# Performance work log

Hardware: AMD Instinct MI355X
Metric: run time of the kernel (lower is better)

## Reference

```python
import jax, jax.numpy as jnp
import numpy as np
import math

B, N, H, TDIM, K, R = 32, 4096, 256, 128, 2, 2


def setup_inputs() -> dict:
    key = jax.random.key(0)
    ks = jax.random.split(key, 12)
    s = 1.0 / math.sqrt(H)
    gain = 1.414
    return {
        "x": jax.random.normal(ks[0], (B, N), jnp.float32),
        "t": jax.random.uniform(ks[1], (B,), jnp.float32),
        # scaled so repeated L@x stays O(1) over Chebyshev hops
        "laplacian": jax.random.normal(ks[2], (N, N), jnp.float32) / math.sqrt(N),
        "w_g1": jax.random.normal(ks[3], (1, H, K + 1), jnp.float32) * gain / math.sqrt(1 + H),
        "w_g2": jax.random.normal(ks[4], (H, 1, K + 1), jnp.float32) * gain / math.sqrt(1 + H),
        "w_t1": jax.random.normal(ks[5], (TDIM, H), jnp.float32) / math.sqrt(TDIM),
        "b_t1": jnp.zeros((H,), jnp.float32),
        "w_t2": jax.random.normal(ks[6], (H, H), jnp.float32) * s,
        "b_t2": jnp.zeros((H,), jnp.float32),
        "w_map": jax.random.normal(ks[7], (N, H), jnp.float32) / math.sqrt(N),
        "b_map": jnp.zeros((H,), jnp.float32),
        "res_w": jax.random.normal(ks[8], (R, 3, H, H), jnp.float32) * s,
        "res_b": jnp.zeros((R, 3, H), jnp.float32),
        "w_o1": jax.random.normal(ks[9], (H, H), jnp.float32) * s,
        "b_o1": jnp.zeros((H,), jnp.float32),
        "w_o2": jax.random.normal(ks[10], (H, N), jnp.float32) * s,
        "b_o2": jnp.zeros((N,), jnp.float32),
    }


def timestep_embedding(t, dim, max_period=10000):
    half = dim // 2  # dim is even here
    freqs = jnp.exp(-math.log(max_period) * jnp.arange(half, dtype=t.dtype) / half)
    args = t[:, None] * freqs[None, :]  # [B, half]
    return jnp.concatenate([jnp.cos(args), jnp.sin(args)], axis=-1)  # [B, dim]


def gcn_layer(L, x, w, conv_order):
    xs = [x]
    h = x
    for _ in range(conv_order):
        h = jnp.einsum('mn,bnc->bmc', L, h)  # sparse-style Laplacian propagation (dense here)
        xs.append(h)
    X = jnp.stack(xs, axis=-1)  # [B, N, C, K+1]
    return jnp.einsum('bnik,iok->bno', X, w)


def reference(x, t, laplacian, w_g1, w_g2, w_t1, b_t1, w_t2, b_t2,
              w_map, b_map, res_w, res_b, w_o1, b_o1, w_o2, b_o2):
    silu = jax.nn.silu
    # time embedding path: sinusoidal -> Linear -> SiLU -> Linear
    temb = timestep_embedding(t, TDIM)
    t_out = silu(temb @ w_t1 + b_t1) @ w_t2 + b_t2  # [B, H]
    # GCNBlock: two Chebyshev GCN layers (GCNLayer.forward applies no activation)
    g = gcn_layer(laplacian, x[:, :, None], w_g1, K)  # [B, N, H]
    g = gcn_layer(laplacian, g, w_g2, K)[..., 0]      # [B, N]
    # ResNet_FC on the node signal
    h = g @ w_map + b_map  # [B, H]
    inv_sqrt2 = 1.0 / math.sqrt(2.0)
    for r in range(R):
        z = h
        for i in range(3):
            z = silu(z @ res_w[r, i] + res_b[r, i])
        h = (h + z) * inv_sqrt2
    # output head with time conditioning
    out = silu((h + t_out) @ w_o1 + b_o1) @ w_o2 + b_o2  # [B, N]
    return out
```

## Files before the change

kernel.cpp:

```cpp
#include <hip/hip_runtime.h>
#include <hip/hip_bf16.h>

typedef __bf16 bf16x8 __attribute__((ext_vector_type(8)));
typedef __bf16 bf16x4 __attribute__((ext_vector_type(4)));
typedef float  f32x4  __attribute__((ext_vector_type(4)));


static constexpr size_t WS_A     = 0;
static constexpr size_t WS_TOUT  = 1024;
static constexpr size_t WS_H0    = 65536;
static constexpr size_t WS_UB    = 131072;
static constexpr size_t WS_XB    = 262144;
static constexpr size_t WS_G2B   = 524288;
static constexpr size_t WS_ZB1   = 1048576;
static constexpr size_t WS_ZBSTR = 262144;
static constexpr size_t WS_Z1    = 2097152;
static constexpr size_t WS_ZSTR  = 524288;
static constexpr size_t WS_WMAPT = 4194304;
static constexpr size_t WS_WO2T  = 6291456;
static constexpr size_t WS_LB    = 8388608;

__device__ __forceinline__ f32x4 mfma16(bf16x8 a, bf16x8 b, f32x4 c) {
    return __builtin_amdgcn_mfma_f32_16x16x32_bf16(a, b, c, 0, 0, 0);
}

__device__ __forceinline__ bf16x8 cvt8(const float* p) {
    f32x4 lo = *(const f32x4*)p;
    f32x4 hi = *(const f32x4*)(p + 4);
    bf16x8 r;
    r[0] = (__bf16)lo[0]; r[1] = (__bf16)lo[1]; r[2] = (__bf16)lo[2]; r[3] = (__bf16)lo[3];
    r[4] = (__bf16)hi[0]; r[5] = (__bf16)hi[1]; r[6] = (__bf16)hi[2]; r[7] = (__bf16)hi[3];
    return r;
}

__device__ __forceinline__ float silu_f(float x) { return x / (1.0f + __expf(-x)); }

__device__ __forceinline__ void transpose_tile(const float* __restrict__ src, int sstride,
                                               __bf16* __restrict__ dst, int dstride,
                                               int r0, int c0, float* sh, int tid) {
    const int r = tid >> 3, cg = (tid & 7) * 4;
    f32x4 v = *(const f32x4*)(src + (size_t)(r0 + r) * sstride + c0 + cg);
    sh[r * 33 + cg + 0] = v[0];
    sh[r * 33 + cg + 1] = v[1];
    sh[r * 33 + cg + 2] = v[2];
    sh[r * 33 + cg + 3] = v[3];
    __syncthreads();
    bf16x4 o;
    o[0] = (__bf16)sh[(cg + 0) * 33 + r];
    o[1] = (__bf16)sh[(cg + 1) * 33 + r];
    o[2] = (__bf16)sh[(cg + 2) * 33 + r];
    o[3] = (__bf16)sh[(cg + 3) * 33 + r];
    *(bf16x4*)(dst + (size_t)(c0 + r) * dstride + r0 + cg) = o;
}

__global__ __launch_bounds__(256) void prep_kernel(
    const float* __restrict__ x, const float* __restrict__ t,
    const float* __restrict__ w_g1, const float* __restrict__ w_g2,
    const float* __restrict__ w_t1, const float* __restrict__ b_t1,
    const float* __restrict__ w_t2, const float* __restrict__ b_t2,
    const float* __restrict__ w_map, const float* __restrict__ w_o2,
    char* __restrict__ ws)
{
    __shared__ float sh[1056];
    const int bi = blockIdx.x, tid = threadIdx.x;
    if (bi == 0) {
        const float g10 = w_g1[tid * 3 + 0], g11 = w_g1[tid * 3 + 1], g12 = w_g1[tid * 3 + 2];
        const float g20 = w_g2[tid * 3 + 0], g21 = w_g2[tid * 3 + 1], g22 = w_g2[tid * 3 + 2];
        float p[9] = {g10 * g20, g10 * g21, g10 * g22,
                      g11 * g20, g11 * g21, g11 * g22,
                      g12 * g20, g12 * g21, g12 * g22};
        const int wv = tid >> 6, ln = tid & 63;
#pragma unroll
        for (int j = 0; j < 9; ++j) {
            float v = p[j];
#pragma unroll
            for (int off = 32; off > 0; off >>= 1) v += __shfl_down(v, off);
            if (ln == 0) sh[wv * 9 + j] = v;
        }
        __syncthreads();
        if (tid == 0) {
            float s[9];
#pragma unroll
            for (int j = 0; j < 9; ++j) s[j] = sh[j] + sh[9 + j] + sh[18 + j] + sh[27 + j];
            float* a = (float*)(ws + WS_A);
            a[0] = s[0];
            a[1] = s[1] + s[3];
            a[2] = s[2] + s[4] + s[6];
            a[3] = s[5] + s[7];
            a[4] = s[8];
        }
    } else if (bi < 33) {
        const int b = bi - 1;
        float* t_out = (float*)(ws + WS_TOUT);
        if (tid < 64) {
            float fr = __expf(-9.210340371976184f * (float)tid * (1.0f / 64.0f));
            float ang = t[b] * fr;
            sh[tid]      = __cosf(ang);
            sh[64 + tid] = __sinf(ang);
        }
        __syncthreads();
        float acc = b_t1[tid];
        for (int j = 0; j < 128; ++j) acc += sh[j] * w_t1[j * 256 + tid];
        sh[128 + tid] = silu_f(acc);
        __syncthreads();
        float acc2 = b_t2[tid];
        for (int j = 0; j < 256; ++j) acc2 += sh[128 + j] * w_t2[j * 256 + tid];
        t_out[b * 256 + tid] = acc2;
    } else if (bi < 41) {
        f32x4* p = (f32x4*)(ws + WS_H0);
        f32x4 z = {0.f, 0.f, 0.f, 0.f};
        p[(bi - 33) * 256 + tid] = z;
    } else if (bi < 105) {
        const int e = ((bi - 41) * 256 + tid) * 8;
        *(bf16x8*)((__bf16*)(ws + WS_XB) + e) = cvt8(x + e);
    } else if (bi < 1129) {
        const int ti = bi - 105;
        transpose_tile(w_map, 256, (__bf16*)(ws + WS_WMAPT), 4096,
                       (ti >> 3) * 32, (ti & 7) * 32, sh, tid);
    } else {
        const int ti = bi - 1129;
        transpose_tile(w_o2, 4096, (__bf16*)(ws + WS_WO2T), 256,
                       (ti & 7) * 32, (ti >> 3) * 32, sh, tid);
    }
}

__global__ __launch_bounds__(1024) void hop1_kernel(
    const float* __restrict__ L, const __bf16* __restrict__ xb,
    float* __restrict__ zout, __bf16* __restrict__ zb_out,
    __bf16* __restrict__ Lb)
{
    __shared__ float red[16][16][33];
    const int bi = blockIdx.x, tid = threadIdx.x;
    const int wave = tid >> 6, lane = tid & 63;
    const int l15 = lane & 15, q = lane >> 4;
    const int m0 = bi * 16;
    const int kbase = wave * 256;

    const float*  lp  = L  + (size_t)(m0 + l15) * 4096;
    __bf16*       lbp = Lb + (size_t)(m0 + l15) * 4096;
    const __bf16* b0p = xb + (size_t)l15 * 4096;
    const __bf16* b1p = xb + (size_t)(l15 + 16) * 4096;

    f32x4 acc0 = {0,0,0,0}, acc1 = {0,0,0,0};
#pragma unroll
    for (int ks = 0; ks < 8; ++ks) {
        const int k = kbase + ks * 32 + q * 8;
        bf16x8 a  = cvt8(lp + k);
        *(bf16x8*)(lbp + k) = a;
        bf16x8 b0 = *(const bf16x8*)(b0p + k);
        bf16x8 b1 = *(const bf16x8*)(b1p + k);
        acc0 = mfma16(a, b0, acc0);
        acc1 = mfma16(a, b1, acc1);
    }
#pragma unroll
    for (int r = 0; r < 4; ++r) {
        red[wave][q * 4 + r][l15]      = acc0[r];
        red[wave][q * 4 + r][l15 + 16] = acc1[r];
    }
    __syncthreads();
    if (tid < 512) {
        const int m = tid & 15, b = tid >> 4;
        float v = 0.f;
#pragma unroll
        for (int w = 0; w < 16; ++w) v += red[w][m][b];
        zout[(size_t)b * 4096 + m0 + m] = v;
        zb_out[(size_t)b * 4096 + m0 + m] = (__bf16)v;
    }
}

__global__ __launch_bounds__(1024) void hop_bf_kernel(
    const __bf16* __restrict__ Lb, const __bf16* __restrict__ zb_in,
    float* __restrict__ zout, __bf16* __restrict__ zb_out)
{
    __shared__ float red[16][16][33];
    const int bi = blockIdx.x, tid = threadIdx.x;
    const int wave = tid >> 6, lane = tid & 63;
    const int l15 = lane & 15, q = lane >> 4;
    const int m0 = bi * 16;
    const int kbase = wave * 256;

    const __bf16* ap  = Lb + (size_t)(m0 + l15) * 4096;
    const __bf16* b0p = zb_in + (size_t)l15 * 4096;
    const __bf16* b1p = zb_in + (size_t)(l15 + 16) * 4096;

    f32x4 acc0 = {0,0,0,0}, acc1 = {0,0,0,0};
#pragma unroll
    for (int ks = 0; ks < 8; ++ks) {
        const int k = kbase + ks * 32 + q * 8;
        bf16x8 a  = *(const bf16x8*)(ap + k);
        bf16x8 b0 = *(const bf16x8*)(b0p + k);
        bf16x8 b1 = *(const bf16x8*)(b1p + k);
        acc0 = mfma16(a, b0, acc0);
        acc1 = mfma16(a, b1, acc1);
    }
#pragma unroll
    for (int r = 0; r < 4; ++r) {
        red[wave][q * 4 + r][l15]      = acc0[r];
        red[wave][q * 4 + r][l15 + 16] = acc1[r];
    }
    __syncthreads();
    if (tid < 512) {
        const int m = tid & 15, b = tid >> 4;
        float v = 0.f;
#pragma unroll
        for (int w = 0; w < 16; ++w) v += red[w][m][b];
        zout[(size_t)b * 4096 + m0 + m] = v;
        if (zb_out) zb_out[(size_t)b * 4096 + m0 + m] = (__bf16)v;
    }
}

__global__ __launch_bounds__(256) void combine_kernel(
    const float* __restrict__ x,
    const float* __restrict__ z1, const float* __restrict__ z2,
    const float* __restrict__ z3, const float* __restrict__ z4,
    const float* __restrict__ a, __bf16* __restrict__ g2b)
{
    const int i = blockIdx.x * 256 + threadIdx.x;
    const float a0 = a[0], a1 = a[1], a2 = a[2], a3 = a[3], a4 = a[4];
    f32x4 r = a0 * ((const f32x4*)x)[i] + a1 * ((const f32x4*)z1)[i]
            + a2 * ((const f32x4*)z2)[i] + a3 * ((const f32x4*)z3)[i]
            + a4 * ((const f32x4*)z4)[i];
    bf16x4 o;
    o[0] = (__bf16)r[0]; o[1] = (__bf16)r[1]; o[2] = (__bf16)r[2]; o[3] = (__bf16)r[3];
    ((bf16x4*)g2b)[i] = o;
}

__global__ __launch_bounds__(256) void map_gemm_kernel(
    const __bf16* __restrict__ g2b, const __bf16* __restrict__ w_mapT,
    float* __restrict__ h0)
{
    __shared__ float red[4][16][32];
    const int bi = blockIdx.x, tid = threadIdx.x;
    const int wave = tid >> 6, lane = tid & 63;
    const int l15 = lane & 15, q = lane >> 4;
    const int btile = bi & 1;
    const int hp = (bi >> 1) & 7;
    const int kc = bi >> 4;
    const int kbase = kc * 512 + wave * 128;

    const __bf16* ap  = g2b + (size_t)(btile * 16 + l15) * 4096;
    const __bf16* bp0 = w_mapT + (size_t)(hp * 32 + l15) * 4096;
    const __bf16* bp1 = w_mapT + (size_t)(hp * 32 + 16 + l15) * 4096;

    f32x4 acc0 = {0,0,0,0}, acc1 = {0,0,0,0};
#pragma unroll
    for (int ks = 0; ks < 4; ++ks) {
        const int k = kbase + ks * 32 + q * 8;
        bf16x8 a  = *(const bf16x8*)(ap + k);
        bf16x8 b0 = *(const bf16x8*)(bp0 + k);
        bf16x8 b1 = *(const bf16x8*)(bp1 + k);
        acc0 = mfma16(a, b0, acc0);
        acc1 = mfma16(a, b1, acc1);
    }
#pragma unroll
    for (int r = 0; r < 4; ++r) {
        red[wave][q * 4 + r][l15]      = acc0[r];
        red[wave][q * 4 + r][l15 + 16] = acc1[r];
    }
    __syncthreads();
    const int b_l = tid >> 4, hl = tid & 15;
#pragma unroll
    for (int s = 0; s < 2; ++s) {
        const int h_l = hl + s * 16;
        float v = red[0][b_l][h_l] + red[1][b_l][h_l] + red[2][b_l][h_l] + red[3][b_l][h_l];
        atomicAdd(h0 + (size_t)(btile * 16 + b_l) * 256 + hp * 32 + h_l, v);
    }
}

__global__ __launch_bounds__(1024) void resnet_kernel(
    const float* __restrict__ h0, const float* __restrict__ b_map,
    const float* __restrict__ res_w, const float* __restrict__ res_b,
    const float* __restrict__ t_out, const float* __restrict__ w_o1,
    const float* __restrict__ b_o1, __bf16* __restrict__ u_b)
{
    __shared__ float zs[256];
    __shared__ float part[4][256];
    const int b = blockIdx.x, tid = threadIdx.x;
    const int col = tid & 255, kg = tid >> 8;

    float hv = 0.f;
    if (kg == 0) {
        hv = h0[b * 256 + col] + b_map[col];
        zs[col] = hv;
    }
    __syncthreads();

#pragma unroll
    for (int r = 0; r < 2; ++r) {
        for (int i = 0; i < 3; ++i) {
            const float* W = res_w + ((size_t)(r * 3 + i) << 16) + (size_t)kg * 64 * 256 + col;
            const float* zp = zs + kg * 64;
            float a0 = 0, a1 = 0, a2 = 0, a3 = 0;
#pragma unroll
            for (int j = 0; j < 64; j += 4) {
                a0 += zp[j]     * W[(j)     * 256];
                a1 += zp[j + 1] * W[(j + 1) * 256];
                a2 += zp[j + 2] * W[(j + 2) * 256];
                a3 += zp[j + 3] * W[(j + 3) * 256];
            }
            part[kg][col] = (a0 + a1) + (a2 + a3);
            __syncthreads();
            if (kg == 0) {
                zs[col] = silu_f(res_b[(r * 3 + i) * 256 + col]
                                 + part[0][col] + part[1][col] + part[2][col] + part[3][col]);
            }
            __syncthreads();
        }
        if (kg == 0) {
            hv = (hv + zs[col]) * 0.70710678118654752f;
            zs[col] = hv;
        }
        __syncthreads();
    }

    if (kg == 0) zs[col] = hv + t_out[b * 256 + col];
    __syncthreads();
    {
        const float* W = w_o1 + (size_t)kg * 64 * 256 + col;
        const float* zp = zs + kg * 64;
        float a0 = 0, a1 = 0, a2 = 0, a3 = 0;
#pragma unroll
        for (int j = 0; j < 64; j += 4) {
            a0 += zp[j]     * W[(j)     * 256];
            a1 += zp[j + 1] * W[(j + 1) * 256];
            a2 += zp[j + 2] * W[(j + 2) * 256];
            a3 += zp[j + 3] * W[(j + 3) * 256];
        }
        part[kg][col] = (a0 + a1) + (a2 + a3);
    }
    __syncthreads();
    if (kg == 0) {
        u_b[b * 256 + col] = (__bf16)silu_f(b_o1[col]
            + part[0][col] + part[1][col] + part[2][col] + part[3][col]);
    }
}

__global__ __launch_bounds__(256) void out_gemm_kernel(
    const __bf16* __restrict__ u_b, const __bf16* __restrict__ w_o2T,
    const float* __restrict__ b_o2, float* __restrict__ out)
{
    const int tid = threadIdx.x;
    const int wave = tid >> 6, lane = tid & 63;
    const int l15 = lane & 15, q = lane >> 4;
    const int g = blockIdx.x * 4 + wave;
    const int btile = g & 1;
    const int n0 = (g >> 1) * 32;

    const __bf16* ap  = u_b + (size_t)(btile * 16 + l15) * 256;
    const __bf16* bp0 = w_o2T + (size_t)(n0 + l15) * 256;
    const __bf16* bp1 = w_o2T + (size_t)(n0 + 16 + l15) * 256;

    f32x4 acc0 = {0,0,0,0}, acc1 = {0,0,0,0};
#pragma unroll
    for (int ks = 0; ks < 8; ++ks) {
        const int k = ks * 32 + q * 8;
        bf16x8 a  = *(const bf16x8*)(ap + k);
        bf16x8 b0 = *(const bf16x8*)(bp0 + k);
        bf16x8 b1 = *(const bf16x8*)(bp1 + k);
        acc0 = mfma16(a, b0, acc0);
        acc1 = mfma16(a, b1, acc1);
    }
    const int row = btile * 16 + q * 4;
    const int na = n0 + l15, nb = n0 + 16 + l15;
#pragma unroll
    for (int r = 0; r < 4; ++r) {
        out[(size_t)(row + r) * 4096 + na] = acc0[r] + b_o2[na];
        out[(size_t)(row + r) * 4096 + nb] = acc1[r] + b_o2[nb];
    }
}

extern "C" void kernel_launch(void* const* d_in, const int* in_sizes, int n_in,
                              void* d_out, int out_size, void* d_ws, size_t ws_size,
                              hipStream_t stream)
{
    (void)in_sizes; (void)n_in; (void)out_size; (void)ws_size;
    const float* x     = (const float*)d_in[0];
    const float* t     = (const float*)d_in[1];
    const float* L     = (const float*)d_in[2];
    const float* w_g1  = (const float*)d_in[3];
    const float* w_g2  = (const float*)d_in[4];
    const float* w_t1  = (const float*)d_in[5];
    const float* b_t1  = (const float*)d_in[6];
    const float* w_t2  = (const float*)d_in[7];
    const float* b_t2  = (const float*)d_in[8];
    const float* w_map = (const float*)d_in[9];
    const float* b_map = (const float*)d_in[10];
    const float* res_w = (const float*)d_in[11];
    const float* res_b = (const float*)d_in[12];
    const float* w_o1  = (const float*)d_in[13];
    const float* b_o1  = (const float*)d_in[14];
    const float* w_o2  = (const float*)d_in[15];
    const float* b_o2  = (const float*)d_in[16];
    float* out = (float*)d_out;
    char* ws = (char*)d_ws;

    float*  a_c  = (float*)(ws + WS_A);
    float*  tout = (float*)(ws + WS_TOUT);
    float*  h0   = (float*)(ws + WS_H0);
    __bf16* u_b  = (__bf16*)(ws + WS_UB);
    __bf16* xb   = (__bf16*)(ws + WS_XB);
    __bf16* g2b  = (__bf16*)(ws + WS_G2B);
    __bf16* zb1  = (__bf16*)(ws + WS_ZB1);
    __bf16* zb2  = (__bf16*)(ws + WS_ZB1 + WS_ZBSTR);
    __bf16* zb3  = (__bf16*)(ws + WS_ZB1 + 2 * WS_ZBSTR);
    float*  z1   = (float*)(ws + WS_Z1);
    float*  z2   = (float*)(ws + WS_Z1 + WS_ZSTR);
    float*  z3   = (float*)(ws + WS_Z1 + 2 * WS_ZSTR);
    float*  z4   = (float*)(ws + WS_Z1 + 3 * WS_ZSTR);
    __bf16* w_mapT = (__bf16*)(ws + WS_WMAPT);
    __bf16* w_o2T  = (__bf16*)(ws + WS_WO2T);
    __bf16* Lb     = (__bf16*)(ws + WS_LB);

    prep_kernel<<<2153, 256, 0, stream>>>(x, t, w_g1, w_g2, w_t1, b_t1, w_t2, b_t2,
                                          w_map, w_o2, ws);
    hop1_kernel<<<256, 1024, 0, stream>>>(L, xb, z1, zb1, Lb);
    hop_bf_kernel<<<256, 1024, 0, stream>>>(Lb, zb1, z2, zb2);
    hop_bf_kernel<<<256, 1024, 0, stream>>>(Lb, zb2, z3, zb3);
    hop_bf_kernel<<<256, 1024, 0, stream>>>(Lb, zb3, z4, nullptr);
    combine_kernel<<<128, 256, 0, stream>>>(x, z1, z2, z3, z4, a_c, g2b);
    map_gemm_kernel<<<128, 256, 0, stream>>>(g2b, w_mapT, h0);
    resnet_kernel<<<32, 1024, 0, stream>>>(h0, b_map, res_w, res_b, tout, w_o1, b_o1, u_b);
    out_gemm_kernel<<<64, 256, 0, stream>>>(u_b, w_o2T, b_o2, out);
}
```

Measured before the change: 229.2 us.

## Fuse Chebyshev hops, combine and map GEMM into one persistent kernel with grid barriers

Six kernels (four Laplacian hops, the combine step and the map GEMM) become one persistent 256-block kernel. Each block keeps its 16-row slice of L in LDS as swizzled bf16, so L is read from HBM once and never written back as a bf16 copy. Hop results stay in registers, and the hops are separated by atomic-counter grid barriers. This removes launch gaps, the round trips of the Lb copy and the fp32 z buffers, and the separate combine pass. The risks are deadlock if all 256 blocks are not co-resident, since 128KB of LDS is used per block, and the cost of the spin barriers.

```diff
diff --git a/kernel.cpp b/kernel.cpp
--- a/kernel.cpp
+++ b/kernel.cpp
@@ -7,18 +7,15 @@
 
 
 static constexpr size_t WS_A     = 0;
+static constexpr size_t WS_BAR   = 512;
 static constexpr size_t WS_TOUT  = 1024;
 static constexpr size_t WS_H0    = 65536;
 static constexpr size_t WS_UB    = 131072;
 static constexpr size_t WS_XB    = 262144;
 static constexpr size_t WS_G2B   = 524288;
-static constexpr size_t WS_ZB1   = 1048576;
-static constexpr size_t WS_ZBSTR = 262144;
-static constexpr size_t WS_Z1    = 2097152;
-static constexpr size_t WS_ZSTR  = 524288;
+static constexpr size_t WS_ZB    = 1048576;
 static constexpr size_t WS_WMAPT = 4194304;
 static constexpr size_t WS_WO2T  = 6291456;
-static constexpr size_t WS_LB    = 8388608;
 
 __device__ __forceinline__ f32x4 mfma16(bf16x8 a, bf16x8 b, f32x4 c) {
     return __builtin_amdgcn_mfma_f32_16x16x32_bf16(a, b, c, 0, 0, 0);
@@ -107,6 +104,7 @@
         for (int j = 0; j < 256; ++j) acc2 += sh[128 + j] * w_t2[j * 256 + tid];
         t_out[b * 256 + tid] = acc2;
     } else if (bi < 41) {
+        if (bi == 33 && tid == 0) *(unsigned*)(ws + WS_BAR) = 0u;
         f32x4* p = (f32x4*)(ws + WS_H0);
         f32x4 z = {0.f, 0.f, 0.f, 0.f};
         p[(bi - 33) * 256 + tid] = z;
@@ -124,146 +122,149 @@
     }
 }
 
-__global__ __launch_bounds__(1024) void hop1_kernel(
-    const float* __restrict__ L, const __bf16* __restrict__ xb,
-    float* __restrict__ zout, __bf16* __restrict__ zb_out,
-    __bf16* __restrict__ Lb)
+__device__ __forceinline__ void gbar(unsigned* bar, unsigned target) {
+    __syncthreads();
+    if (threadIdx.x == 0) {
+        __threadfence();
+        __hip_atomic_fetch_add(bar, 1u, __ATOMIC_RELEASE, __HIP_MEMORY_SCOPE_AGENT);
+        while (__hip_atomic_load(bar, __ATOMIC_RELAXED, __HIP_MEMORY_SCOPE_AGENT) < target)
+            __builtin_amdgcn_s_sleep(2);
+        (void)__hip_atomic_load(bar, __ATOMIC_ACQUIRE, __HIP_MEMORY_SCOPE_AGENT);
+    }
+    __syncthreads();
+}
+
+__global__ __launch_bounds__(1024) void cheb_fused(
+    const float* __restrict__ L, const float* __restrict__ x, char* __restrict__ ws)
 {
-    __shared__ float red[16][16][33];
+    __shared__ __bf16 lb[16 * 4096];
+    __shared__ float red[8][16][33];
+
+    unsigned* bar        = (unsigned*)(ws + WS_BAR);
+    const float* a_c     = (const float*)(ws + WS_A);
+    const __bf16* xb     = (const __bf16*)(ws + WS_XB);
+    const __bf16* w_mapT = (const __bf16*)(ws + WS_WMAPT);
+    __bf16* g2b          = (__bf16*)(ws + WS_G2B);
+    __bf16* zb1          = (__bf16*)(ws + WS_ZB);
+    __bf16* zb2          = zb1 + 131072;
+    __bf16* zb3          = zb2 + 131072;
+    float* h0            = (float*)(ws + WS_H0);
+
     const int bi = blockIdx.x, tid = threadIdx.x;
     const int wave = tid >> 6, lane = tid & 63;
     const int l15 = lane & 15, q = lane >> 4;
     const int m0 = bi * 16;
-    const int kbase = wave * 256;
-
-    const float*  lp  = L  + (size_t)(m0 + l15) * 4096;
-    __bf16*       lbp = Lb + (size_t)(m0 + l15) * 4096;
-    const __bf16* b0p = xb + (size_t)l15 * 4096;
-    const __bf16* b1p = xb + (size_t)(l15 + 16) * 4096;
-
-    f32x4 acc0 = {0,0,0,0}, acc1 = {0,0,0,0};
-#pragma unroll
-    for (int ks = 0; ks < 8; ++ks) {
-        const int k = kbase + ks * 32 + q * 8;
-        bf16x8 a  = cvt8(lp + k);
-        *(bf16x8*)(lbp + k) = a;
-        bf16x8 b0 = *(const bf16x8*)(b0p + k);
-        bf16x8 b1 = *(const bf16x8*)(b1p + k);
-        acc0 = mfma16(a, b0, acc0);
-        acc1 = mfma16(a, b1, acc1);
-    }
-#pragma unroll
-    for (int r = 0; r < 4; ++r) {
-        red[wave][q * 4 + r][l15]      = acc0[r];
-        red[wave][q * 4 + r][l15 + 16] = acc1[r];
-    }
-    __syncthreads();
+
+    {
+        const int cb = tid * 8;
+#pragma unroll
+        for (int i = 0; i < 16; ++i) {
+            f32x4 v = *(const f32x4*)(L + (size_t)(m0 + i) * 4096 + tid * 4);
+            bf16x4 o;
+            o[0] = (__bf16)v[0]; o[1] = (__bf16)v[1];
+            o[2] = (__bf16)v[2]; o[3] = (__bf16)v[3];
+            *(bf16x4*)((char*)lb + i * 8192 + (cb ^ ((i & 7) << 4))) = o;
+        }
+    }
+    __syncthreads();
+
+    const int xr = (l15 & 7) << 4;
+    const char* arow = (const char*)lb + l15 * 8192;
+    const int kb0 = wave * 512 + q * 16;
+
+    float z1v, z2v, z3v, z4v;
+
+    auto hop = [&](const __bf16* bsrc, __bf16* zb_out, float& zv) {
+        const __bf16* b0p = bsrc + (size_t)l15 * 4096;
+        const __bf16* b1p = bsrc + (size_t)(l15 + 16) * 4096;
+        f32x4 acc0 = {0,0,0,0}, acc1 = {0,0,0,0};
+#pragma unroll
+        for (int ks = 0; ks < 8; ++ks) {
+            const int kbyte = kb0 + ks * 64;
+            bf16x8 a = *(const bf16x8*)(arow + (kbyte ^ xr));
+            const int k = kbyte >> 1;
+            bf16x8 b0 = *(const bf16x8*)(b0p + k);
+            bf16x8 b1 = *(const bf16x8*)(b1p + k);
+            acc0 = mfma16(a, b0, acc0);
+            acc1 = mfma16(a, b1, acc1);
+        }
+        if (wave >= 8) {
+#pragma unroll
+            for (int r = 0; r < 4; ++r) {
+                red[wave - 8][q * 4 + r][l15]      = acc0[r];
+                red[wave - 8][q * 4 + r][l15 + 16] = acc1[r];
+            }
+        }
+        __syncthreads();
+        if (wave < 8) {
+#pragma unroll
+            for (int r = 0; r < 4; ++r) {
+                red[wave][q * 4 + r][l15]      += acc0[r];
+                red[wave][q * 4 + r][l15 + 16] += acc1[r];
+            }
+        }
+        __syncthreads();
+        float v = 0.f;
+        if (tid < 512) {
+            const int m = tid & 15, b = tid >> 4;
+#pragma unroll
+            for (int w = 0; w < 8; ++w) v += red[w][m][b];
+            if (zb_out) zb_out[(size_t)b * 4096 + m0 + m] = (__bf16)v;
+        }
+        zv = v;
+    };
+
+    hop(xb, zb1, z1v);
+    gbar(bar, 256u);
+    hop(zb1, zb2, z2v);
+    gbar(bar, 512u);
+    hop(zb2, zb3, z3v);
+    gbar(bar, 768u);
+    hop(zb3, nullptr, z4v);
+
     if (tid < 512) {
         const int m = tid & 15, b = tid >> 4;
-        float v = 0.f;
-#pragma unroll
-        for (int w = 0; w < 16; ++w) v += red[w][m][b];
-        zout[(size_t)b * 4096 + m0 + m] = v;
-        zb_out[(size_t)b * 4096 + m0 + m] = (__bf16)v;
-    }
-}
-
-__global__ __launch_bounds__(1024) void hop_bf_kernel(
-    const __bf16* __restrict__ Lb, const __bf16* __restrict__ zb_in,
-    float* __restrict__ zout, __bf16* __restrict__ zb_out)
-{
-    __shared__ float red[16][16][33];
-    const int bi = blockIdx.x, tid = threadIdx.x;
-    const int wave = tid >> 6, lane = tid & 63;
-    const int l15 = lane & 15, q = lane >> 4;
-    const int m0 = bi * 16;
-    const int kbase = wave * 256;
-
-    const __bf16* ap  = Lb + (size_t)(m0 + l15) * 4096;
-    const __bf16* b0p = zb_in + (size_t)l15 * 4096;
-    const __bf16* b1p = zb_in + (size_t)(l15 + 16) * 4096;
-
-    f32x4 acc0 = {0,0,0,0}, acc1 = {0,0,0,0};
-#pragma unroll
-    for (int ks = 0; ks < 8; ++ks) {
-        const int k = kbase + ks * 32 + q * 8;
-        bf16x8 a  = *(const bf16x8*)(ap + k);
-        bf16x8 b0 = *(const bf16x8*)(b0p + k);
-        bf16x8 b1 = *(const bf16x8*)(b1p + k);
-        acc0 = mfma16(a, b0, acc0);
-        acc1 = mfma16(a, b1, acc1);
-    }
-#pragma unroll
-    for (int r = 0; r < 4; ++r) {
-        red[wave][q * 4 + r][l15]      = acc0[r];
-        red[wave][q * 4 + r][l15 + 16] = acc1[r];
-    }
-    __syncthreads();
-    if (tid < 512) {
-        const int m = tid & 15, b = tid >> 4;
-        float v = 0.f;
-#pragma unroll
-        for (int w = 0; w < 16; ++w) v += red[w][m][b];
-        zout[(size_t)b * 4096 + m0 + m] = v;
-        if (zb_out) zb_out[(size_t)b * 4096 + m0 + m] = (__bf16)v;
-    }
-}
-
-__global__ __launch_bounds__(256) void combine_kernel(
-    const float* __restrict__ x,
-    const float* __restrict__ z1, const float* __restrict__ z2,
-    const float* __restrict__ z3, const float* __restrict__ z4,
-    const float* __restrict__ a, __bf16* __restrict__ g2b)
-{
-    const int i = blockIdx.x * 256 + threadIdx.x;
-    const float a0 = a[0], a1 = a[1], a2 = a[2], a3 = a[3], a4 = a[4];
-    f32x4 r = a0 * ((const f32x4*)x)[i] + a1 * ((const f32x4*)z1)[i]
-            + a2 * ((const f32x4*)z2)[i] + a3 * ((const f32x4*)z3)[i]
-            + a4 * ((const f32x4*)z4)[i];
-    bf16x4 o;
-    o[0] = (__bf16)r[0]; o[1] = (__bf16)r[1]; o[2] = (__bf16)r[2]; o[3] = (__bf16)r[3];
-    ((bf16x4*)g2b)[i] = o;
-}
-
-__global__ __launch_bounds__(256) void map_gemm_kernel(
-    const __bf16* __restrict__ g2b, const __bf16* __restrict__ w_mapT,
-    float* __restrict__ h0)
-{
-    __shared__ float red[4][16][32];
-    const int bi = blockIdx.x, tid = threadIdx.x;
-    const int wave = tid >> 6, lane = tid & 63;
-    const int l15 = lane & 15, q = lane >> 4;
-    const int btile = bi & 1;
-    const int hp = (bi >> 1) & 7;
-    const int kc = bi >> 4;
-    const int kbase = kc * 512 + wave * 128;
-
-    const __bf16* ap  = g2b + (size_t)(btile * 16 + l15) * 4096;
-    const __bf16* bp0 = w_mapT + (size_t)(hp * 32 + l15) * 4096;
-    const __bf16* bp1 = w_mapT + (size_t)(hp * 32 + 16 + l15) * 4096;
-
-    f32x4 acc0 = {0,0,0,0}, acc1 = {0,0,0,0};
-#pragma unroll
-    for (int ks = 0; ks < 4; ++ks) {
-        const int k = kbase + ks * 32 + q * 8;
-        bf16x8 a  = *(const bf16x8*)(ap + k);
-        bf16x8 b0 = *(const bf16x8*)(bp0 + k);
-        bf16x8 b1 = *(const bf16x8*)(bp1 + k);
-        acc0 = mfma16(a, b0, acc0);
-        acc1 = mfma16(a, b1, acc1);
-    }
-#pragma unroll
-    for (int r = 0; r < 4; ++r) {
-        red[wave][q * 4 + r][l15]      = acc0[r];
-        red[wave][q * 4 + r][l15 + 16] = acc1[r];
-    }
-    __syncthreads();
-    const int b_l = tid >> 4, hl = tid & 15;
-#pragma unroll
-    for (int s = 0; s < 2; ++s) {
-        const int h_l = hl + s * 16;
-        float v = red[0][b_l][h_l] + red[1][b_l][h_l] + red[2][b_l][h_l] + red[3][b_l][h_l];
-        atomicAdd(h0 + (size_t)(btile * 16 + b_l) * 256 + hp * 32 + h_l, v);
+        const float xv = x[(size_t)b * 4096 + m0 + m];
+        const float g = a_c[0] * xv + a_c[1] * z1v + a_c[2] * z2v
+                      + a_c[3] * z3v + a_c[4] * z4v;
+        g2b[(size_t)b * 4096 + m0 + m] = (__bf16)g;
+    }
+    gbar(bar, 1024u);
+
+    {
+        const int btile = bi & 1, hp = (bi >> 1) & 7, kc = bi >> 4;
+        if (wave < 4) {
+            const int kbase = kc * 256 + wave * 64;
+            const __bf16* ap  = g2b + (size_t)(btile * 16 + l15) * 4096;
+            const __bf16* bp0 = w_mapT + (size_t)(hp * 32 + l15) * 4096;
+            const __bf16* bp1 = w_mapT + (size_t)(hp * 32 + 16 + l15) * 4096;
+            f32x4 acc0 = {0,0,0,0}, acc1 = {0,0,0,0};
+#pragma unroll
+            for (int ks = 0; ks < 2; ++ks) {
+                const int k = kbase + ks * 32 + q * 8;
+                bf16x8 a  = *(const bf16x8*)(ap + k);
+                bf16x8 b0 = *(const bf16x8*)(bp0 + k);
+                bf16x8 b1 = *(const bf16x8*)(bp1 + k);
+                acc0 = mfma16(a, b0, acc0);
+                acc1 = mfma16(a, b1, acc1);
+            }
+#pragma unroll
+            for (int r = 0; r < 4; ++r) {
+                red[wave][q * 4 + r][l15]      = acc0[r];
+                red[wave][q * 4 + r][l15 + 16] = acc1[r];
+            }
+        }
+        __syncthreads();
+        if (tid < 256) {
+            const int b_l = tid >> 4, hl = tid & 15;
+#pragma unroll
+            for (int s = 0; s < 2; ++s) {
+                const int h_l = hl + s * 16;
+                const float v = red[0][b_l][h_l] + red[1][b_l][h_l]
+                              + red[2][b_l][h_l] + red[3][b_l][h_l];
+                atomicAdd(h0 + (size_t)(btile * 16 + b_l) * 256 + hp * 32 + h_l, v);
+            }
+        }
     }
 }
 
@@ -394,31 +395,14 @@
     float* out = (float*)d_out;
     char* ws = (char*)d_ws;
 
-    float*  a_c  = (float*)(ws + WS_A);
     float*  tout = (float*)(ws + WS_TOUT);
     float*  h0   = (float*)(ws + WS_H0);
     __bf16* u_b  = (__bf16*)(ws + WS_UB);
-    __bf16* xb   = (__bf16*)(ws + WS_XB);
-    __bf16* g2b  = (__bf16*)(ws + WS_G2B);
-    __bf16* zb1  = (__bf16*)(ws + WS_ZB1);
-    __bf16* zb2  = (__bf16*)(ws + WS_ZB1 + WS_ZBSTR);
-    __bf16* zb3  = (__bf16*)(ws + WS_ZB1 + 2 * WS_ZBSTR);
-    float*  z1   = (float*)(ws + WS_Z1);
-    float*  z2   = (float*)(ws + WS_Z1 + WS_ZSTR);
-    float*  z3   = (float*)(ws + WS_Z1 + 2 * WS_ZSTR);
-    float*  z4   = (float*)(ws + WS_Z1 + 3 * WS_ZSTR);
-    __bf16* w_mapT = (__bf16*)(ws + WS_WMAPT);
-    __bf16* w_o2T  = (__bf16*)(ws + WS_WO2T);
-    __bf16* Lb     = (__bf16*)(ws + WS_LB);
+    __bf16* w_o2T = (__bf16*)(ws + WS_WO2T);
 
     prep_kernel<<<2153, 256, 0, stream>>>(x, t, w_g1, w_g2, w_t1, b_t1, w_t2, b_t2,
                                           w_map, w_o2, ws);
-    hop1_kernel<<<256, 1024, 0, stream>>>(L, xb, z1, zb1, Lb);
-    hop_bf_kernel<<<256, 1024, 0, stream>>>(Lb, zb1, z2, zb2);
-    hop_bf_kernel<<<256, 1024, 0, stream>>>(Lb, zb2, z3, zb3);
-    hop_bf_kernel<<<256, 1024, 0, stream>>>(Lb, zb3, z4, nullptr);
-    combine_kernel<<<128, 256, 0, stream>>>(x, z1, z2, z3, z4, a_c, g2b);
-    map_gemm_kernel<<<128, 256, 0, stream>>>(g2b, w_mapT, h0);
+    cheb_fused<<<256, 1024, 0, stream>>>(L, x, ws);
     resnet_kernel<<<32, 1024, 0, stream>>>(h0, b_map, res_w, res_b, tout, w_o1, b_o1, u_b);
     out_gemm_kernel<<<64, 256, 0, stream>>>(u_b, w_o2T, b_o2, out);
 }
```

Result: slower. 286.7 us (+25.1%).

## Prefetch hop loads into registers, fuse combine into last hop, vectorize resnet

Applied to the files above, without the earlier changes.

Hop kernels now issue all their global loads up front, or double-buffer them in hop1, so more memory requests are in flight before the MFMAs run. The separate combine kernel is folded into the fourth hop's epilogue, which removes one launch and the write and reread of z4. The resnet kernel is reorganized into 16 k-groups using f32x4 weight loads through a shared layer lambda. Launch bounds with min-blocks hints are added, which raises register pressure from the larger prefetch arrays.

```diff
diff --git a/kernel.cpp b/kernel.cpp
--- a/kernel.cpp
+++ b/kernel.cpp
@@ -12,10 +12,10 @@
 static constexpr size_t WS_UB    = 131072;
 static constexpr size_t WS_XB    = 262144;
 static constexpr size_t WS_G2B   = 524288;
-static constexpr size_t WS_ZB1   = 1048576;
+static constexpr size_t WS_ZB    = 1048576;
 static constexpr size_t WS_ZBSTR = 262144;
-static constexpr size_t WS_Z1    = 2097152;
-static constexpr size_t WS_ZSTR  = 524288;
+static constexpr size_t WS_ZF    = 2097152;
+static constexpr size_t WS_ZFSTR = 524288;
 static constexpr size_t WS_WMAPT = 4194304;
 static constexpr size_t WS_WO2T  = 6291456;
 static constexpr size_t WS_LB    = 8388608;
@@ -124,9 +124,9 @@
     }
 }
 
-__global__ __launch_bounds__(1024) void hop1_kernel(
+__global__ __launch_bounds__(1024, 4) void hop1_kernel(
     const float* __restrict__ L, const __bf16* __restrict__ xb,
-    float* __restrict__ zout, __bf16* __restrict__ zb_out,
+    float* __restrict__ zf_out, __bf16* __restrict__ zb_out,
     __bf16* __restrict__ Lb)
 {
     __shared__ float red[16][16][33];
@@ -134,23 +134,46 @@
     const int wave = tid >> 6, lane = tid & 63;
     const int l15 = lane & 15, q = lane >> 4;
     const int m0 = bi * 16;
-    const int kbase = wave * 256;
+    const int kbase = wave * 256 + q * 8;
 
     const float*  lp  = L  + (size_t)(m0 + l15) * 4096;
     __bf16*       lbp = Lb + (size_t)(m0 + l15) * 4096;
     const __bf16* b0p = xb + (size_t)l15 * 4096;
     const __bf16* b1p = xb + (size_t)(l15 + 16) * 4096;
 
+    f32x4 af0[4], af1[4];
+    bf16x8 b0r[4], b1r[4];
+#pragma unroll
+    for (int p = 0; p < 4; ++p) {
+        const int k = kbase + p * 32;
+        af0[p] = *(const f32x4*)(lp + k);
+        af1[p] = *(const f32x4*)(lp + k + 4);
+        b0r[p] = *(const bf16x8*)(b0p + k);
+        b1r[p] = *(const bf16x8*)(b1p + k);
+    }
+
     f32x4 acc0 = {0,0,0,0}, acc1 = {0,0,0,0};
 #pragma unroll
     for (int ks = 0; ks < 8; ++ks) {
-        const int k = kbase + ks * 32 + q * 8;
-        bf16x8 a  = cvt8(lp + k);
-        *(bf16x8*)(lbp + k) = a;
-        bf16x8 b0 = *(const bf16x8*)(b0p + k);
-        bf16x8 b1 = *(const bf16x8*)(b1p + k);
-        acc0 = mfma16(a, b0, acc0);
-        acc1 = mfma16(a, b1, acc1);
+        const int p = ks & 3;
+        bf16x8 a;
+        a[0] = (__bf16)af0[p][0]; a[1] = (__bf16)af0[p][1];
+        a[2] = (__bf16)af0[p][2]; a[3] = (__bf16)af0[p][3];
+        a[4] = (__bf16)af1[p][0]; a[5] = (__bf16)af1[p][1];
+        a[6] = (__bf16)af1[p][2]; a[7] = (__bf16)af1[p][3];
+        *(bf16x8*)(lbp + kbase + ks * 32) = a;
+        if (ks < 4) {
+            const int k2 = kbase + (ks + 4) * 32;
+            af0[p] = *(const f32x4*)(lp + k2);
+            af1[p] = *(const f32x4*)(lp + k2 + 4);
+            acc0 = mfma16(a, b0r[p], acc0);
+            acc1 = mfma16(a, b1r[p], acc1);
+            b0r[p] = *(const bf16x8*)(b0p + k2);
+            b1r[p] = *(const bf16x8*)(b1p + k2);
+        } else {
+            acc0 = mfma16(a, b0r[p], acc0);
+            acc1 = mfma16(a, b1r[p], acc1);
+        }
     }
 #pragma unroll
     for (int r = 0; r < 4; ++r) {
@@ -163,35 +186,39 @@
         float v = 0.f;
 #pragma unroll
         for (int w = 0; w < 16; ++w) v += red[w][m][b];
-        zout[(size_t)b * 4096 + m0 + m] = v;
+        zf_out[(size_t)b * 4096 + m0 + m] = v;
         zb_out[(size_t)b * 4096 + m0 + m] = (__bf16)v;
     }
 }
 
-__global__ __launch_bounds__(1024) void hop_bf_kernel(
+__global__ __launch_bounds__(1024, 4) void hop_mid_kernel(
     const __bf16* __restrict__ Lb, const __bf16* __restrict__ zb_in,
-    float* __restrict__ zout, __bf16* __restrict__ zb_out)
+    float* __restrict__ zf_out, __bf16* __restrict__ zb_out)
 {
     __shared__ float red[16][16][33];
     const int bi = blockIdx.x, tid = threadIdx.x;
     const int wave = tid >> 6, lane = tid & 63;
     const int l15 = lane & 15, q = lane >> 4;
     const int m0 = bi * 16;
-    const int kbase = wave * 256;
+    const int kbase = wave * 256 + q * 8;
 
     const __bf16* ap  = Lb + (size_t)(m0 + l15) * 4096;
     const __bf16* b0p = zb_in + (size_t)l15 * 4096;
     const __bf16* b1p = zb_in + (size_t)(l15 + 16) * 4096;
 
+    bf16x8 ar[8], b0r[8], b1r[8];
+#pragma unroll
+    for (int ks = 0; ks < 8; ++ks) {
+        const int k = kbase + ks * 32;
+        ar[ks]  = *(const bf16x8*)(ap + k);
+        b0r[ks] = *(const bf16x8*)(b0p + k);
+        b1r[ks] = *(const bf16x8*)(b1p + k);
+    }
     f32x4 acc0 = {0,0,0,0}, acc1 = {0,0,0,0};
 #pragma unroll
     for (int ks = 0; ks < 8; ++ks) {
-        const int k = kbase + ks * 32 + q * 8;
-        bf16x8 a  = *(const bf16x8*)(ap + k);
-        bf16x8 b0 = *(const bf16x8*)(b0p + k);
-        bf16x8 b1 = *(const bf16x8*)(b1p + k);
-        acc0 = mfma16(a, b0, acc0);
-        acc1 = mfma16(a, b1, acc1);
+        acc0 = mfma16(ar[ks], b0r[ks], acc0);
+        acc1 = mfma16(ar[ks], b1r[ks], acc1);
     }
 #pragma unroll
     for (int r = 0; r < 4; ++r) {
@@ -204,25 +231,59 @@
         float v = 0.f;
 #pragma unroll
         for (int w = 0; w < 16; ++w) v += red[w][m][b];
-        zout[(size_t)b * 4096 + m0 + m] = v;
-        if (zb_out) zb_out[(size_t)b * 4096 + m0 + m] = (__bf16)v;
-    }
-}
-
-__global__ __launch_bounds__(256) void combine_kernel(
+        zf_out[(size_t)b * 4096 + m0 + m] = v;
+        zb_out[(size_t)b * 4096 + m0 + m] = (__bf16)v;
+    }
+}
+
+__global__ __launch_bounds__(1024, 4) void hop4_kernel(
+    const __bf16* __restrict__ Lb, const __bf16* __restrict__ zb_in,
     const float* __restrict__ x,
-    const float* __restrict__ z1, const float* __restrict__ z2,
-    const float* __restrict__ z3, const float* __restrict__ z4,
-    const float* __restrict__ a, __bf16* __restrict__ g2b)
-{
-    const int i = blockIdx.x * 256 + threadIdx.x;
-    const float a0 = a[0], a1 = a[1], a2 = a[2], a3 = a[3], a4 = a[4];
-    f32x4 r = a0 * ((const f32x4*)x)[i] + a1 * ((const f32x4*)z1)[i]
-            + a2 * ((const f32x4*)z2)[i] + a3 * ((const f32x4*)z3)[i]
-            + a4 * ((const f32x4*)z4)[i];
-    bf16x4 o;
-    o[0] = (__bf16)r[0]; o[1] = (__bf16)r[1]; o[2] = (__bf16)r[2]; o[3] = (__bf16)r[3];
-    ((bf16x4*)g2b)[i] = o;
+    const float* __restrict__ z1f, const float* __restrict__ z2f,
+    const float* __restrict__ z3f, const float* __restrict__ a_c,
+    __bf16* __restrict__ g2b)
+{
+    __shared__ float red[16][16][33];
+    const int bi = blockIdx.x, tid = threadIdx.x;
+    const int wave = tid >> 6, lane = tid & 63;
+    const int l15 = lane & 15, q = lane >> 4;
+    const int m0 = bi * 16;
+    const int kbase = wave * 256 + q * 8;
+
+    const __bf16* ap  = Lb + (size_t)(m0 + l15) * 4096;
+    const __bf16* b0p = zb_in + (size_t)l15 * 4096;
+    const __bf16* b1p = zb_in + (size_t)(l15 + 16) * 4096;
+
+    bf16x8 ar[8], b0r[8], b1r[8];
+#pragma unroll
+    for (int ks = 0; ks < 8; ++ks) {
+        const int k = kbase + ks * 32;
+        ar[ks]  = *(const bf16x8*)(ap + k);
+        b0r[ks] = *(const bf16x8*)(b0p + k);
+        b1r[ks] = *(const bf16x8*)(b1p + k);
+    }
+    f32x4 acc0 = {0,0,0,0}, acc1 = {0,0,0,0};
+#pragma unroll
+    for (int ks = 0; ks < 8; ++ks) {
+        acc0 = mfma16(ar[ks], b0r[ks], acc0);
+        acc1 = mfma16(ar[ks], b1r[ks], acc1);
+    }
+#pragma unroll
+    for (int r = 0; r < 4; ++r) {
+        red[wave][q * 4 + r][l15]      = acc0[r];
+        red[wave][q * 4 + r][l15 + 16] = acc1[r];
+    }
+    __syncthreads();
+    if (tid < 512) {
+        const int m = tid & 15, b = tid >> 4;
+        float v = 0.f;
+#pragma unroll
+        for (int w = 0; w < 16; ++w) v += red[w][m][b];
+        const size_t idx = (size_t)b * 4096 + m0 + m;
+        const float g = a_c[0] * x[idx] + a_c[1] * z1f[idx] + a_c[2] * z2f[idx]
+                      + a_c[3] * z3f[idx] + a_c[4] * v;
+        g2b[idx] = (__bf16)g;
+    }
 }
 
 __global__ __launch_bounds__(256) void map_gemm_kernel(
@@ -267,72 +328,58 @@
     }
 }
 
-__global__ __launch_bounds__(1024) void resnet_kernel(
+__global__ __launch_bounds__(1024, 4) void resnet_kernel(
     const float* __restrict__ h0, const float* __restrict__ b_map,
     const float* __restrict__ res_w, const float* __restrict__ res_b,
     const float* __restrict__ t_out, const float* __restrict__ w_o1,
     const float* __restrict__ b_o1, __bf16* __restrict__ u_b)
 {
     __shared__ float zs[256];
-    __shared__ float part[4][256];
+    __shared__ float part[16][256];
     const int b = blockIdx.x, tid = threadIdx.x;
-    const int col = tid & 255, kg = tid >> 8;
+    const int kg = tid >> 6, c4 = (tid & 63) * 4;
 
     float hv = 0.f;
-    if (kg == 0) {
-        hv = h0[b * 256 + col] + b_map[col];
-        zs[col] = hv;
-    }
-    __syncthreads();
+    if (tid < 256) {
+        hv = h0[b * 256 + tid] + b_map[tid];
+        zs[tid] = hv;
+    }
+    __syncthreads();
+
+    auto layer = [&](const float* __restrict__ Wbase, const float* __restrict__ bias,
+                     bool to_u) {
+        const float* W = Wbase + (size_t)(kg * 16) * 256 + c4;
+        const float* zp = zs + kg * 16;
+        f32x4 acc = {0.f, 0.f, 0.f, 0.f};
+#pragma unroll
+        for (int j = 0; j < 16; ++j) acc += zp[j] * *(const f32x4*)(W + (size_t)j * 256);
+        *(f32x4*)&part[kg][c4] = acc;
+        __syncthreads();
+        if (tid < 256) {
+            float s = bias[tid];
+#pragma unroll
+            for (int g = 0; g < 16; ++g) s += part[g][tid];
+            s = silu_f(s);
+            if (to_u) u_b[b * 256 + tid] = (__bf16)s;
+            else zs[tid] = s;
+        }
+        __syncthreads();
+    };
 
 #pragma unroll
     for (int r = 0; r < 2; ++r) {
-        for (int i = 0; i < 3; ++i) {
-            const float* W = res_w + ((size_t)(r * 3 + i) << 16) + (size_t)kg * 64 * 256 + col;
-            const float* zp = zs + kg * 64;
-            float a0 = 0, a1 = 0, a2 = 0, a3 = 0;
-#pragma unroll
-            for (int j = 0; j < 64; j += 4) {
-                a0 += zp[j]     * W[(j)     * 256];
-                a1 += zp[j + 1] * W[(j + 1) * 256];
-                a2 += zp[j + 2] * W[(j + 2) * 256];
-                a3 += zp[j + 3] * W[(j + 3) * 256];
-            }
-            part[kg][col] = (a0 + a1) + (a2 + a3);
-            __syncthreads();
-            if (kg == 0) {
-                zs[col] = silu_f(res_b[(r * 3 + i) * 256 + col]
-                                 + part[0][col] + part[1][col] + part[2][col] + part[3][col]);
-            }
-            __syncthreads();
-        }
-        if (kg == 0) {
-            hv = (hv + zs[col]) * 0.70710678118654752f;
-            zs[col] = hv;
-        }
-        __syncthreads();
-    }
-
-    if (kg == 0) zs[col] = hv + t_out[b * 256 + col];
-    __syncthreads();
-    {
-        const float* W = w_o1 + (size_t)kg * 64 * 256 + col;
-        const float* zp = zs + kg * 64;
-        float a0 = 0, a1 = 0, a2 = 0, a3 = 0;
-#pragma unroll
-        for (int j = 0; j < 64; j += 4) {
-            a0 += zp[j]     * W[(j)     * 256];
-            a1 += zp[j + 1] * W[(j + 1) * 256];
-            a2 += zp[j + 2] * W[(j + 2) * 256];
-            a3 += zp[j + 3] * W[(j + 3) * 256];
-        }
-        part[kg][col] = (a0 + a1) + (a2 + a3);
-    }
-    __syncthreads();
-    if (kg == 0) {
-        u_b[b * 256 + col] = (__bf16)silu_f(b_o1[col]
-            + part[0][col] + part[1][col] + part[2][col] + part[3][col]);
-    }
+        for (int i = 0; i < 3; ++i)
+            layer(res_w + ((size_t)(r * 3 + i) << 16), res_b + (r * 3 + i) * 256, false);
+        if (tid < 256) {
+            hv = (hv + zs[tid]) * 0.70710678118654752f;
+            zs[tid] = hv;
+        }
+        __syncthreads();
+    }
+
+    if (tid < 256) zs[tid] = hv + t_out[b * 256 + tid];
+    __syncthreads();
+    layer(w_o1, b_o1, true);
 }
 
 __global__ __launch_bounds__(256) void out_gemm_kernel(
@@ -400,24 +447,22 @@
     __bf16* u_b  = (__bf16*)(ws + WS_UB);
     __bf16* xb   = (__bf16*)(ws + WS_XB);
     __bf16* g2b  = (__bf16*)(ws + WS_G2B);
-    __bf16* zb1  = (__bf16*)(ws + WS_ZB1);
-    __bf16* zb2  = (__bf16*)(ws + WS_ZB1 + WS_ZBSTR);
-    __bf16* zb3  = (__bf16*)(ws + WS_ZB1 + 2 * WS_ZBSTR);
-    float*  z1   = (float*)(ws + WS_Z1);
-    float*  z2   = (float*)(ws + WS_Z1 + WS_ZSTR);
-    float*  z3   = (float*)(ws + WS_Z1 + 2 * WS_ZSTR);
-    float*  z4   = (float*)(ws + WS_Z1 + 3 * WS_ZSTR);
+    __bf16* zb1  = (__bf16*)(ws + WS_ZB);
+    __bf16* zb2  = zb1 + 131072;
+    __bf16* zb3  = zb2 + 131072;
+    float*  z1f  = (float*)(ws + WS_ZF);
+    float*  z2f  = z1f + 131072;
+    float*  z3f  = z2f + 131072;
     __bf16* w_mapT = (__bf16*)(ws + WS_WMAPT);
     __bf16* w_o2T  = (__bf16*)(ws + WS_WO2T);
     __bf16* Lb     = (__bf16*)(ws + WS_LB);
 
     prep_kernel<<<2153, 256, 0, stream>>>(x, t, w_g1, w_g2, w_t1, b_t1, w_t2, b_t2,
                                           w_map, w_o2, ws);
-    hop1_kernel<<<256, 1024, 0, stream>>>(L, xb, z1, zb1, Lb);
-    hop_bf_kernel<<<256, 1024, 0, stream>>>(Lb, zb1, z2, zb2);
-    hop_bf_kernel<<<256, 1024, 0, stream>>>(Lb, zb2, z3, zb3);
-    hop_bf_kernel<<<256, 1024, 0, stream>>>(Lb, zb3, z4, nullptr);
-    combine_kernel<<<128, 256, 0, stream>>>(x, z1, z2, z3, z4, a_c, g2b);
+    hop1_kernel<<<256, 1024, 0, stream>>>(L, xb, z1f, zb1, Lb);
+    hop_mid_kernel<<<256, 1024, 0, stream>>>(Lb, zb1, z2f, zb2);
+    hop_mid_kernel<<<256, 1024, 0, stream>>>(Lb, zb2, z3f, zb3);
+    hop4_kernel<<<256, 1024, 0, stream>>>(Lb, zb3, x, z1f, z2f, z3f, a_c, g2b);
     map_gemm_kernel<<<128, 256, 0, stream>>>(g2b, w_mapT, h0);
     resnet_kernel<<<32, 1024, 0, stream>>>(h0, b_map, res_w, res_b, tout, w_o1, b_o1, u_b);
     out_gemm_kernel<<<64, 256, 0, stream>>>(u_b, w_o2T, b_o2, out);
```

Result: slower. 240.3 us (+4.9%).
